# Optimization experiments

Hardware: AMD Instinct MI355X
Metric: run time of the kernel (lower is better)

Reference implementation:

```python
import jax, jax.numpy as jnp
import numpy as np

NUM_EMBEDDINGS = 4096
EMBEDDING_DIM = 64
COMMITMENT_COST = 0.25
DECAY = 0.99
EPSILON = 1e-05


def setup_inputs() -> dict:
    key = jax.random.key(0)
    k1, k2, k3, k4 = jax.random.split(key, 4)
    z = jax.random.normal(k1, (128, 24, 1536), dtype=jnp.float32)
    embedding = jax.random.normal(k2, (NUM_EMBEDDINGS, EMBEDDING_DIM), dtype=jnp.float32) * 0.05
    ema_cluster_size = jax.random.uniform(k3, (NUM_EMBEDDINGS,), dtype=jnp.float32)
    ema_w = jax.random.normal(k4, (NUM_EMBEDDINGS, EMBEDDING_DIM), dtype=jnp.float32) * 0.05
    return {"z": z, "embedding": embedding, "ema_cluster_size": ema_cluster_size, "ema_w": ema_w}


def reference(z, embedding, ema_cluster_size, ema_w):
    # VectorQuantizer.forward in training mode (EMA codebook update).
    K, d = embedding.shape
    B = z.shape[0]
    z_flat = z.reshape(-1, d)  # [N, d], N = B*576

    # Pairwise squared distances: ||z||^2 + ||e||^2 - 2 z e^T  -> [N, K]
    dist = (jnp.sum(z_flat * z_flat, axis=1, keepdims=True)
            + jnp.sum(embedding * embedding, axis=1)
            - 2.0 * (z_flat @ embedding.T))
    codes = jnp.argmin(dist, axis=1)  # [N]

    # EMA statistics (one-hot scatter expressed as segment sums)
    counts = jax.ops.segment_sum(jnp.ones_like(codes, dtype=z.dtype), codes, num_segments=K)
    new_cluster_size = DECAY * ema_cluster_size + (1.0 - DECAY) * counts
    dw = jax.ops.segment_sum(z_flat, codes, num_segments=K)  # [K, d]
    new_ema_w = DECAY * ema_w + (1.0 - DECAY) * dw

    n = jnp.sum(new_cluster_size)
    cluster_size = (new_cluster_size + EPSILON) / (n + K * EPSILON) * n
    new_embedding = new_ema_w / cluster_size[:, None]

    # Quantize with the UPDATED codebook (torch copies weights before embedding lookup)
    z_q = new_embedding[codes].reshape(z.shape)
    vq_loss = COMMITMENT_COST * jnp.mean((jax.lax.stop_gradient(z_q) - z) ** 2)
    z_q_st = z + jax.lax.stop_gradient(z_q - z)  # straight-through
    codes = codes.reshape(B, -1)  # [B, 576]
    return (vq_loss, z_q_st, codes, new_embedding, new_cluster_size, new_ema_w)
```

## Files before the change

kernel.cpp:

```cpp
#include <hip/hip_runtime.h>

constexpr int KC    = 4096;
constexpr int DIM   = 64;
constexpr int NROWS = 73728;
constexpr int NELEM = 4718592;
constexpr int GSTRIDE = 4160;

typedef _Float16 f16x8 __attribute__((ext_vector_type(8)));
typedef float    f32x4 __attribute__((ext_vector_type(4)));

constexpr size_t OUT_LOSS  = 0;
constexpr size_t OUT_ZQ    = 1;
constexpr size_t OUT_CODES = 1 + (size_t)NELEM;
constexpr size_t OUT_EMB   = OUT_CODES + (size_t)NROWS;
constexpr size_t OUT_NCS   = OUT_EMB + (size_t)KC * DIM;
constexpr size_t OUT_NEW   = OUT_NCS + (size_t)KC;

constexpr size_t alignup(size_t x, size_t a) { return (x + a - 1) & ~(a - 1); }
constexpr size_t WS_CODES  = 0;
constexpr size_t WS_COUNTS = WS_CODES + sizeof(int) * (size_t)NROWS;
constexpr size_t WS_OFFS   = WS_COUNTS + sizeof(int) * (size_t)KC;
constexpr size_t WS_CURSOR = alignup(WS_OFFS + sizeof(int) * (KC + 1), 16);
constexpr size_t WS_SORTED = WS_CURSOR + sizeof(int) * (size_t)KC;
constexpr size_t WS_N      = alignup(WS_SORTED + sizeof(int) * (size_t)NROWS, 16);
constexpr size_t WS_LOSSD  = alignup(WS_N + sizeof(float), 8);
constexpr size_t WS_EMBPK  = alignup(WS_LOSSD + 8, 64);

__global__ void k_prep(const float* __restrict__ emb, char* __restrict__ emb_pk,
                       int* __restrict__ counts) {
    if (threadIdx.x < 32) counts[blockIdx.x * 32 + threadIdx.x] = 0;
    int t = blockIdx.x * 256 + threadIdx.x;
    int c = t >> 3, q = t & 7;
    const float* ep = emb + (size_t)c * DIM + q * 8;
    f16x8 hv, lv;
    float s = 0.f;
    #pragma unroll
    for (int e = 0; e < 8; ++e) {
        float x = ep[e];
        _Float16 h = (_Float16)x;
        float r = x - (float)h;
        hv[e] = h;
        lv[e] = (_Float16)(r * 2048.0f);
        s = fmaf(x, x, s);
    }
    s += __shfl_xor(s, 1, 64);
    s += __shfl_xor(s, 2, 64);
    s += __shfl_xor(s, 4, 64);
    int g = c >> 4, lc = c & 15;
    int h = q >> 2, lq = q & 3;
    int lane = lq * 16 + lc;
    char* gbase = emb_pk + (size_t)g * GSTRIDE;
    if (q == 0) *(float*)(gbase + lc * 4) = 1024.0f * s;
    char* base = gbase + 64 + lane * 16;
    *(f16x8*)(base + h * 1024)       = hv;
    *(f16x8*)(base + (2 + h) * 1024) = lv;
}

__global__ __launch_bounds__(192, 2) void k_argmin7(
        const float* __restrict__ z, const char* __restrict__ emb_pk,
        int* __restrict__ codes_i, float* __restrict__ codes_f,
        int* __restrict__ counts) {
    __shared__ int codebuf[3][48];

    const int tid = threadIdx.x;
    const int l   = tid & 63;
    const int w   = tid >> 6;
    const int lc  = l & 15;
    const int lq  = l >> 4;
    const int waveRow = blockIdx.x * 144 + w * 48;

    f16x8 ah2k[3][2], ahr[3][2], al2k[3][2];
    #pragma unroll
    for (int rt = 0; rt < 3; ++rt)
        #pragma unroll
        for (int h = 0; h < 2; ++h) {
            const float* zp = z + (size_t)(waveRow + rt * 16 + lc) * DIM + h * 32 + lq * 8;
            float4 x0 = *(const float4*)zp;
            float4 x1 = *(const float4*)(zp + 4);
            float xs[8] = {x0.x, x0.y, x0.z, x0.w, x1.x, x1.y, x1.z, x1.w};
            #pragma unroll
            for (int e = 0; e < 8; ++e) {
                _Float16 hh = (_Float16)xs[e];
                float rr = xs[e] - (float)hh;
                ahr[rt][h][e]  = -hh;
                ah2k[rt][h][e] = (_Float16)(-2048.0f * (float)hh);
                al2k[rt][h][e] = -(_Float16)(rr * 2048.0f);
            }
        }

    float best[3][4];
    int   bestg[3][4];
    #pragma unroll
    for (int rt = 0; rt < 3; ++rt)
        #pragma unroll
        for (int j = 0; j < 4; ++j) { best[rt][j] = INFINITY; bestg[rt][j] = 0; }

    const unsigned long long pkb = (unsigned long long)emb_pk;
    unsigned voffA = 64 + l * 16;
    unsigned voffB = lc * 4;

    f16x8 b00, b01, b02, b03, b10, b11, b12, b13;
    f16x8 b20, b21, b22, b23, b30, b31, b32, b33;
    float e0, e1, e2v, e3;

#define ISSUE(B0, B1, B2, B3, EV)                                                        \
    asm volatile("global_load_dword %0, %1, %2"             : "=v"(EV) : "v"(voffB), "s"(pkb)); \
    asm volatile("global_load_dwordx4 %0, %1, %2"             : "=v"(B0) : "v"(voffA), "s"(pkb)); \
    asm volatile("global_load_dwordx4 %0, %1, %2 offset:1024" : "=v"(B1) : "v"(voffA), "s"(pkb)); \
    asm volatile("global_load_dwordx4 %0, %1, %2 offset:2048" : "=v"(B2) : "v"(voffA), "s"(pkb)); \
    asm volatile("global_load_dwordx4 %0, %1, %2 offset:3072" : "=v"(B3) : "v"(voffA), "s"(pkb)); \
    voffA += GSTRIDE; voffB += GSTRIDE;

#define WAITP                                                \
    asm volatile("s_waitcnt vmcnt(15)" ::: "memory");        \
    __builtin_amdgcn_sched_barrier(0);

#define COMP(B0, B1, B2, B3, EV, G) {                                             \
        f32x4 ci; ci[0] = EV; ci[1] = EV; ci[2] = EV; ci[3] = EV;                 \
        _Pragma("unroll")                                                         \
        for (int rt = 0; rt < 3; ++rt) {                                          \
            f32x4 acc = __builtin_amdgcn_mfma_f32_16x16x32_f16(ah2k[rt][0], B0, ci, 0, 0, 0); \
            acc = __builtin_amdgcn_mfma_f32_16x16x32_f16(ah2k[rt][1], B1, acc, 0, 0, 0);      \
            acc = __builtin_amdgcn_mfma_f32_16x16x32_f16(ahr[rt][0],  B2, acc, 0, 0, 0);      \
            acc = __builtin_amdgcn_mfma_f32_16x16x32_f16(ahr[rt][1],  B3, acc, 0, 0, 0);      \
            acc = __builtin_amdgcn_mfma_f32_16x16x32_f16(al2k[rt][0], B0, acc, 0, 0, 0);      \
            acc = __builtin_amdgcn_mfma_f32_16x16x32_f16(al2k[rt][1], B1, acc, 0, 0, 0);      \
            _Pragma("unroll")                                                     \
            for (int j = 0; j < 4; ++j) {                                         \
                if (acc[j] < best[rt][j]) { best[rt][j] = acc[j]; bestg[rt][j] = (G); } \
            }                                                                     \
        } }

    __builtin_amdgcn_sched_barrier(0);
    ISSUE(b00, b01, b02, b03, e0)
    ISSUE(b10, b11, b12, b13, e1)
    ISSUE(b20, b21, b22, b23, e2v)
    ISSUE(b30, b31, b32, b33, e3)

    for (int g = 0; g < 256; g += 4) {
        WAITP  COMP(b00, b01, b02, b03, e0,  g)      ISSUE(b00, b01, b02, b03, e0)
        WAITP  COMP(b10, b11, b12, b13, e1,  g + 1)  ISSUE(b10, b11, b12, b13, e1)
        WAITP  COMP(b20, b21, b22, b23, e2v, g + 2)  ISSUE(b20, b21, b22, b23, e2v)
        WAITP  COMP(b30, b31, b32, b33, e3,  g + 3)  ISSUE(b30, b31, b32, b33, e3)
    }
    asm volatile("s_waitcnt vmcnt(0)" ::: "memory");
    __builtin_amdgcn_sched_barrier(0);
#undef ISSUE
#undef WAITP
#undef COMP

    #pragma unroll
    for (int rt = 0; rt < 3; ++rt)
        #pragma unroll
        for (int j = 0; j < 4; ++j) {
            float b = best[rt][j];
            int   k = bestg[rt][j] * 16 + lc;
            #pragma unroll
            for (int m = 1; m < 16; m <<= 1) {
                float obv = __shfl_xor(b, m, 64);
                int   okv = __shfl_xor(k, m, 64);
                if (obv < b || (obv == b && okv < k)) { b = obv; k = okv; }
            }
            if (lc == 0) codebuf[w][rt * 16 + lq * 4 + j] = k;
        }

    if (l < 48) {
        int code = codebuf[w][l];
        size_t rowg = (size_t)waveRow + l;
        codes_i[rowg] = code;
        codes_f[rowg] = (float)code;
        atomicAdd(&counts[code], 1);
    }
}

__global__ void k_scan(const int* __restrict__ counts,
                       int* __restrict__ offsets, int* __restrict__ cursor,
                       const float* __restrict__ ema_cs, float* __restrict__ ncs_out,
                       float* __restrict__ n_out, double* __restrict__ lossp) {
    __shared__ int   part[256];
    __shared__ float fpart[256];
    int tid = threadIdx.x;
    if (tid == 0) *lossp = 0.0;
    int base = tid * 16;
    int loc[16];
    int s = 0;
    float fs = 0.f;
    #pragma unroll
    for (int j = 0; j < 16; ++j) {
        int cnt = counts[base + j];
        loc[j] = s; s += cnt;
        float v = 0.99f * ema_cs[base + j] + 0.01f * (float)cnt;
        ncs_out[base + j] = v;
        fs += v;
    }
    part[tid] = s;
    fpart[tid] = fs;
    __syncthreads();
    for (int off = 1; off < 256; off <<= 1) {
        int v = (tid >= off) ? part[tid - off] : 0;
        __syncthreads();
        part[tid] += v;
        __syncthreads();
    }
    int excl = part[tid] - s;
    #pragma unroll
    for (int j = 0; j < 16; ++j) {
        int o = excl + loc[j];
        offsets[base + j] = o;
        cursor[base + j]  = o;
    }
    if (tid == 255) offsets[KC] = excl + s;
    for (int m = 128; m > 0; m >>= 1) {
        if (tid < m) fpart[tid] += fpart[tid + m];
        __syncthreads();
    }
    if (tid == 0) n_out[0] = fpart[0];
}

__global__ void k_scatteridx(const int* __restrict__ codes_i,
                             int* __restrict__ cursor, int* __restrict__ sorted_rows) {
    int r = blockIdx.x * 256 + threadIdx.x;
    if (r < NROWS) {
        int c = codes_i[r];
        int p = atomicAdd(&cursor[c], 1);
        sorted_rows[p] = r;
    }
}

__global__ __launch_bounds__(64) void k_dwsum(
        const float* __restrict__ z, const int* __restrict__ offsets,
        const int* __restrict__ sorted_rows, const float* __restrict__ ema_w,
        const float* __restrict__ ncs, const float* __restrict__ nptr,
        float* __restrict__ new_ema_w_out, float* __restrict__ new_emb_out) {
    int k = blockIdx.x, tid = threadIdx.x;
    int beg = offsets[k], end = offsets[k + 1];
    float a0 = 0.f, a1 = 0.f, a2 = 0.f, a3 = 0.f;
    int i = beg;
    for (; i + 3 < end; i += 4) {
        int r0 = sorted_rows[i], r1 = sorted_rows[i + 1];
        int r2 = sorted_rows[i + 2], r3 = sorted_rows[i + 3];
        a0 += z[(size_t)r0 * DIM + tid];
        a1 += z[(size_t)r1 * DIM + tid];
        a2 += z[(size_t)r2 * DIM + tid];
        a3 += z[(size_t)r3 * DIM + tid];
    }
    for (; i < end; ++i) a0 += z[(size_t)sorted_rows[i] * DIM + tid];
    float dwv = (a0 + a1) + (a2 + a3);
    size_t idx = (size_t)k * DIM + tid;
    float n = nptr[0];
    float nw = 0.99f * ema_w[idx] + 0.01f * dwv;
    float cs = (ncs[k] + 1e-5f) / (n + 4096.0f * 1e-5f) * n;
    new_ema_w_out[idx] = nw;
    new_emb_out[idx] = nw / cs;
}

__global__ __launch_bounds__(256) void k_quant(
        const float* __restrict__ z, const float* __restrict__ new_emb,
        const int* __restrict__ codes, float* __restrict__ zq_out,
        double* __restrict__ loss_acc) {
    __shared__ double red[256];
    const int nvec = NELEM / 4;
    int t = blockIdx.x * 256 + threadIdx.x;
    int stride = gridDim.x * 256;
    double ls = 0.0;
    for (int v = t; v < nvec; v += stride) {
        int e0 = v * 4;
        int n  = e0 >> 6;
        int d0 = e0 & 63;
        int code = codes[n];
        float4 zq = *(const float4*)&new_emb[(size_t)code * DIM + d0];
        float4 zv = *(const float4*)&z[e0];
        float dx = zq.x - zv.x, dy = zq.y - zv.y, dz = zq.z - zv.z, dw4 = zq.w - zv.w;
        float4 o;
        o.x = zv.x + dx; o.y = zv.y + dy; o.z = zv.z + dz; o.w = zv.w + dw4;
        *(float4*)&zq_out[e0] = o;
        ls += (double)(dx * dx) + (double)(dy * dy) + (double)(dz * dz) + (double)(dw4 * dw4);
    }
    red[threadIdx.x] = ls;
    __syncthreads();
    for (int m = 128; m > 0; m >>= 1) {
        if (threadIdx.x < m) red[threadIdx.x] += red[threadIdx.x + m];
        __syncthreads();
    }
    if (threadIdx.x == 0) atomicAdd(loss_acc, red[0]);
}

__global__ void k_loss(const double* __restrict__ loss_acc, float* __restrict__ out0) {
    out0[0] = (float)(0.25 * (loss_acc[0] / (double)NELEM));
}

extern "C" void kernel_launch(void* const* d_in, const int* in_sizes, int n_in,
                              void* d_out, int out_size, void* d_ws, size_t ws_size,
                              hipStream_t stream) {
    const float* z      = (const float*)d_in[0];
    const float* emb    = (const float*)d_in[1];
    const float* ema_cs = (const float*)d_in[2];
    const float* ema_w  = (const float*)d_in[3];
    float* out = (float*)d_out;
    char*  ws  = (char*)d_ws;

    int*    codes_i = (int*)(ws + WS_CODES);
    int*    counts  = (int*)(ws + WS_COUNTS);
    int*    offsets = (int*)(ws + WS_OFFS);
    int*    cursor  = (int*)(ws + WS_CURSOR);
    int*    sorted  = (int*)(ws + WS_SORTED);
    float*  nptr    = (float*)(ws + WS_N);
    double* lossp   = (double*)(ws + WS_LOSSD);
    char*   emb_pk  = ws + WS_EMBPK;

    k_prep<<<(KC * 8) / 256, 256, 0, stream>>>(emb, emb_pk, counts);
    k_argmin7<<<NROWS / 144, 192, 0, stream>>>(z, emb_pk, codes_i,
                                               out + OUT_CODES, counts);
    k_scan<<<1, 256, 0, stream>>>(counts, offsets, cursor, ema_cs,
                                  out + OUT_NCS, nptr, lossp);
    k_scatteridx<<<(NROWS + 255) / 256, 256, 0, stream>>>(codes_i, cursor, sorted);
    k_dwsum<<<KC, 64, 0, stream>>>(z, offsets, sorted, ema_w,
                                   out + OUT_NCS, nptr, out + OUT_NEW, out + OUT_EMB);
    k_quant<<<1152, 256, 0, stream>>>(z, out + OUT_EMB, codes_i,
                                      out + OUT_ZQ, lossp);
    k_loss<<<1, 1, 0, stream>>>(lossp, out + OUT_LOSS);
}
```

Baseline: 167.6 us.

## Fuse loss finalize into quant kernel and make argmin loop branchless

Drops the separate single-thread loss kernel by having the last k_quant block, found through an atomic ticket, compute the final loss, which saves one launch. The argmin inner update becomes branchless select/fminf, the main loop is kept rolled (unroll 1), and the prefetch offsets wrap back to the start on the last iteration so the tail prefetch stays in bounds. A rolled loop may add loop overhead, and the in-loop reset check adds a branch.

```diff
diff --git a/kernel.cpp b/kernel.cpp
--- a/kernel.cpp
+++ b/kernel.cpp
@@ -23,7 +23,8 @@
 constexpr size_t WS_CURSOR = alignup(WS_OFFS + sizeof(int) * (KC + 1), 16);
 constexpr size_t WS_SORTED = WS_CURSOR + sizeof(int) * (size_t)KC;
 constexpr size_t WS_N      = alignup(WS_SORTED + sizeof(int) * (size_t)NROWS, 16);
-constexpr size_t WS_LOSSD  = alignup(WS_N + sizeof(float), 8);
+constexpr size_t WS_TICKET = WS_N + sizeof(float);
+constexpr size_t WS_LOSSD  = alignup(WS_TICKET + sizeof(int), 8);
 constexpr size_t WS_EMBPK  = alignup(WS_LOSSD + 8, 64);
 
 __global__ void k_prep(const float* __restrict__ emb, char* __restrict__ emb_pk,
@@ -56,7 +57,7 @@
     *(f16x8*)(base + (2 + h) * 1024) = lv;
 }
 
-__global__ __launch_bounds__(192, 2) void k_argmin7(
+__global__ __launch_bounds__(192, 2) void k_argmin14(
         const float* __restrict__ z, const char* __restrict__ emb_pk,
         int* __restrict__ codes_i, float* __restrict__ codes_f,
         int* __restrict__ counts) {
@@ -96,8 +97,10 @@
         for (int j = 0; j < 4; ++j) { best[rt][j] = INFINITY; bestg[rt][j] = 0; }
 
     const unsigned long long pkb = (unsigned long long)emb_pk;
-    unsigned voffA = 64 + l * 16;
-    unsigned voffB = lc * 4;
+    const unsigned voffA0 = 64 + l * 16;
+    const unsigned voffB0 = lc * 4;
+    unsigned voffA = voffA0;
+    unsigned voffB = voffB0;
 
     f16x8 b00, b01, b02, b03, b10, b11, b12, b13;
     f16x8 b20, b21, b22, b23, b30, b31, b32, b33;
@@ -127,7 +130,8 @@
             acc = __builtin_amdgcn_mfma_f32_16x16x32_f16(al2k[rt][1], B1, acc, 0, 0, 0);      \
             _Pragma("unroll")                                                     \
             for (int j = 0; j < 4; ++j) {                                         \
-                if (acc[j] < best[rt][j]) { best[rt][j] = acc[j]; bestg[rt][j] = (G); } \
+                bestg[rt][j] = (acc[j] < best[rt][j]) ? (G) : bestg[rt][j];       \
+                best[rt][j]  = fminf(best[rt][j], acc[j]);                        \
             }                                                                     \
         } }
 
@@ -137,7 +141,9 @@
     ISSUE(b20, b21, b22, b23, e2v)
     ISSUE(b30, b31, b32, b33, e3)
 
+    #pragma unroll 1
     for (int g = 0; g < 256; g += 4) {
+        if (g == 252) { voffA = voffA0; voffB = voffB0; }
         WAITP  COMP(b00, b01, b02, b03, e0,  g)      ISSUE(b00, b01, b02, b03, e0)
         WAITP  COMP(b10, b11, b12, b13, e1,  g + 1)  ISSUE(b10, b11, b12, b13, e1)
         WAITP  COMP(b20, b21, b22, b23, e2v, g + 2)  ISSUE(b20, b21, b22, b23, e2v)
@@ -176,11 +182,12 @@
 __global__ void k_scan(const int* __restrict__ counts,
                        int* __restrict__ offsets, int* __restrict__ cursor,
                        const float* __restrict__ ema_cs, float* __restrict__ ncs_out,
-                       float* __restrict__ n_out, double* __restrict__ lossp) {
+                       float* __restrict__ n_out, double* __restrict__ lossp,
+                       int* __restrict__ ticket) {
     __shared__ int   part[256];
     __shared__ float fpart[256];
     int tid = threadIdx.x;
-    if (tid == 0) *lossp = 0.0;
+    if (tid == 0) { *lossp = 0.0; *ticket = 0; }
     int base = tid * 16;
     int loc[16];
     int s = 0;
@@ -257,7 +264,8 @@
 __global__ __launch_bounds__(256) void k_quant(
         const float* __restrict__ z, const float* __restrict__ new_emb,
         const int* __restrict__ codes, float* __restrict__ zq_out,
-        double* __restrict__ loss_acc) {
+        double* __restrict__ loss_acc, int* __restrict__ ticket,
+        float* __restrict__ out0, int nblocks) {
     __shared__ double red[256];
     const int nvec = NELEM / 4;
     int t = blockIdx.x * 256 + threadIdx.x;
@@ -282,11 +290,15 @@
         if (threadIdx.x < m) red[threadIdx.x] += red[threadIdx.x + m];
         __syncthreads();
     }
-    if (threadIdx.x == 0) atomicAdd(loss_acc, red[0]);
-}
-
-__global__ void k_loss(const double* __restrict__ loss_acc, float* __restrict__ out0) {
-    out0[0] = (float)(0.25 * (loss_acc[0] / (double)NELEM));
+    if (threadIdx.x == 0) {
+        atomicAdd(loss_acc, red[0]);
+        __threadfence();
+        int tk = atomicAdd(ticket, 1);
+        if (tk == nblocks - 1) {
+            double L = atomicAdd(loss_acc, 0.0);
+            out0[0] = (float)(0.25 * (L / (double)NELEM));
+        }
+    }
 }
 
 extern "C" void kernel_launch(void* const* d_in, const int* in_sizes, int n_in,
@@ -305,18 +317,19 @@
     int*    cursor  = (int*)(ws + WS_CURSOR);
     int*    sorted  = (int*)(ws + WS_SORTED);
     float*  nptr    = (float*)(ws + WS_N);
+    int*    ticket  = (int*)(ws + WS_TICKET);
     double* lossp   = (double*)(ws + WS_LOSSD);
     char*   emb_pk  = ws + WS_EMBPK;
 
     k_prep<<<(KC * 8) / 256, 256, 0, stream>>>(emb, emb_pk, counts);
-    k_argmin7<<<NROWS / 144, 192, 0, stream>>>(z, emb_pk, codes_i,
-                                               out + OUT_CODES, counts);
+    k_argmin14<<<NROWS / 144, 192, 0, stream>>>(z, emb_pk, codes_i,
+                                                out + OUT_CODES, counts);
     k_scan<<<1, 256, 0, stream>>>(counts, offsets, cursor, ema_cs,
-                                  out + OUT_NCS, nptr, lossp);
+                                  out + OUT_NCS, nptr, lossp, ticket);
     k_scatteridx<<<(NROWS + 255) / 256, 256, 0, stream>>>(codes_i, cursor, sorted);
     k_dwsum<<<KC, 64, 0, stream>>>(z, offsets, sorted, ema_w,
                                    out + OUT_NCS, nptr, out + OUT_NEW, out + OUT_EMB);
     k_quant<<<1152, 256, 0, stream>>>(z, out + OUT_EMB, codes_i,
-                                      out + OUT_ZQ, lossp);
-    k_loss<<<1, 1, 0, stream>>>(lossp, out + OUT_LOSS);
-}
+                                      out + OUT_ZQ, lossp, ticket,
+                                      out + OUT_LOSS, 1152);
+}
```

Result: slower. 200.0 us (+19.4%).
